# Optimization experiments

Hardware: AMD Instinct MI355X
Metric: run time of the kernel (lower is better)

Reference implementation:

```python
import jax, jax.numpy as jnp
import numpy as np

E = 16          # number of experts
K = 2           # top-k routing
D = 1024        # model dim
F = 512         # expert ffn dim
T = 4096        # tokens
C = 2048


def setup_inputs() -> dict:
    key = jax.random.key(0)
    k1, k2, k3, k4, k5, k6 = jax.random.split(key, 6)
    return {
        "hidden_states": jax.random.normal(k1, (T, D), jnp.float32),
        "topk_indices": jax.random.randint(k2, (T, K), 0, E, jnp.int64),
        "topk_weights": jax.random.uniform(k3, (T, K), jnp.float32),
        "w_gate": jax.random.normal(k4, (E, D, F), jnp.float32) * 0.02,
        "w_up": jax.random.normal(k5, (E, D, F), jnp.float32) * 0.02,
        "w_down": jax.random.normal(k6, (E, F, D), jnp.float32) * 0.02,
    }


def reference(hidden_states, topk_indices, topk_weights, w_gate, w_up, w_down):
    Tn, d = hidden_states.shape
    k = topk_indices.shape[1]
    TK = Tn * k

    # ---- dispatch_tokens: group (token, expert) pairs by expert id ----
    flat_e = topk_indices.reshape(-1)                 # [TK] expert id per slot
    flat_w = topk_weights.reshape(-1)                 # [TK]
    flat_t = jnp.arange(TK) // k                      # [TK] source token id
    order = jnp.argsort(flat_e)                       # sort slots by expert
    se, st, sw = flat_e[order], flat_t[order], flat_w[order]
    counts = jnp.bincount(flat_e, length=E)           # tokens per expert
    starts = jnp.cumsum(counts) - counts              # exclusive prefix sum
    pos = jnp.arange(TK) - starts[se]                 # position within expert bucket
    valid = pos < C
    slot = jnp.where(valid, se * C + pos, E * C)      # overflow -> scratch row

    # gather tokens into padded per-expert buffers [E, C, D]
    buf = jnp.zeros((E * C + 1, d), hidden_states.dtype).at[slot].set(hidden_states[st])
    xe = buf[: E * C].reshape(E, C, d)

    # ---- per-expert gated-SiLU MLP via grouped GEMMs ----
    h = jax.nn.silu(jnp.einsum('ecd,edf->ecf', xe, w_gate)) * jnp.einsum('ecd,edf->ecf', xe, w_up)
    ye = jnp.einsum('ecf,efd->ecd', h, w_down).reshape(E * C, d)

    # ---- weighted scatter-add combine (index_add_) ----
    contrib = ye[jnp.minimum(slot, E * C - 1)] * (sw * valid.astype(sw.dtype))[:, None]
    out = jnp.zeros((Tn, d), topk_weights.dtype).at[st].add(contrib)
    return out.astype(hidden_states.dtype)
```

## Files before the change

### kernel.cpp

```cpp
#include <hip/hip_runtime.h>
#include <hip/hip_bf16.h>

constexpr int E_ = 16, K_ = 2, D_ = 1024, F_ = 512, T_ = 4096;
constexpr int TK_ = T_ * K_;
constexpr int CAP_ = 2048;
constexpr int BM_ = 128;
constexpr int ROWS_MAX = 10240;

constexpr size_t SZ_W   = (size_t)E_ * F_ * D_ * 2;
constexpr size_t OFF_WDT  = 0;
constexpr size_t OFF_WGT  = OFF_WDT + SZ_W;
constexpr size_t OFF_WUT  = OFF_WGT + SZ_W;
constexpr size_t OFF_XG   = OFF_WUT + SZ_W;
constexpr size_t SZ_XG  = (size_t)ROWS_MAX * D_ * 2;
constexpr size_t OFF_H    = OFF_XG + SZ_XG;
constexpr size_t SZ_H   = (size_t)ROWS_MAX * F_ * 2;
constexpr size_t OFF_META = OFF_H + SZ_H;
constexpr size_t OFF_YE   = OFF_WGT;
static_assert(OFF_YE + (size_t)ROWS_MAX * D_ * 4 <= OFF_H, "Ye overlaps live buffers");

typedef __attribute__((ext_vector_type(8))) short short8;
typedef __attribute__((ext_vector_type(4))) float float4v;

__device__ __forceinline__ unsigned short f2bf(float f) {
  union { float f; unsigned int u; } v; v.f = f;
  unsigned int r = (v.u + 0x7fffu + ((v.u >> 16) & 1u)) >> 16;
  return (unsigned short)r;
}

__device__ __forceinline__ void load_lds16(const unsigned short* g, unsigned short* l) {
  __builtin_amdgcn_global_load_lds(
      (const __attribute__((address_space(1))) unsigned int*)g,
      (__attribute__((address_space(3))) unsigned int*)l,
      16, 0, 0);
}

__launch_bounds__(1024)
__global__ void dispatch_k(const int* __restrict__ idx, const float* __restrict__ tw,
                           int* __restrict__ cnt_c, int* __restrict__ off_al,
                           int* __restrict__ row_token, float* __restrict__ row_weight,
                           int* __restrict__ slot_row) {
  __shared__ int hist[E_], offs[E_], ctr[E_];
  int tid = threadIdx.x;
  if (tid < E_) hist[tid] = 0;
  __syncthreads();
  for (int i = tid; i < TK_; i += 1024) atomicAdd(&hist[idx[i]], 1);
  __syncthreads();
  if (tid == 0) {
    int run = 0;
    for (int e = 0; e < E_; ++e) {
      int c = hist[e] > CAP_ ? CAP_ : hist[e];
      cnt_c[e] = c; off_al[e] = run; offs[e] = run; ctr[e] = 0;
      run += (c + BM_ - 1) & ~(BM_ - 1);
    }
  }
  __syncthreads();
  for (int r = tid; r < ROWS_MAX; r += 1024) row_token[r] = -1;
  __syncthreads();
  for (int i = tid; i < TK_; i += 1024) {
    int e = idx[i];
    int r = atomicAdd(&ctr[e], 1);
    int row = -1;
    if (r < CAP_) {
      row = offs[e] + r;
      row_token[row] = i >> 1;
      row_weight[row] = tw[i];
    }
    slot_row[i] = row;
  }
}

__global__ void gather_k(const float* __restrict__ hidden, const int* __restrict__ row_token,
                         unsigned short* __restrict__ Xg) {
  int r = blockIdx.x;
  int tok = row_token[r];
  int c = threadIdx.x * 4;
  ushort4 o;
  if (tok >= 0) {
    float4 v = *(const float4*)(hidden + (size_t)tok * D_ + c);
    o.x = f2bf(v.x); o.y = f2bf(v.y); o.z = f2bf(v.z); o.w = f2bf(v.w);
  } else {
    o.x = 0; o.y = 0; o.z = 0; o.w = 0;
  }
  *(ushort4*)(Xg + (size_t)r * D_ + c) = o;
}

__launch_bounds__(256)
__global__ void transpose_all_k(const float* __restrict__ wg, const float* __restrict__ wu,
                                const float* __restrict__ wd,
                                unsigned short* __restrict__ WgT, unsigned short* __restrict__ WuT,
                                unsigned short* __restrict__ WdT) {
  __shared__ float tile[64][65];
  int z = blockIdx.y;
  int kind = z >> 4, e = z & 15;
  int R = (kind == 2) ? F_ : D_;
  int C = (kind == 2) ? D_ : F_;
  const float* s = ((kind == 0) ? wg : (kind == 1) ? wu : wd) + (size_t)e * R * C;
  unsigned short* d = ((kind == 0) ? WgT : (kind == 1) ? WuT : WdT) + (size_t)e * R * C;
  int tilesX = C >> 6;
  int t = blockIdx.x;
  int r0 = (t / tilesX) * 64, c0 = (t % tilesX) * 64;

  int lr = threadIdx.x >> 4;
  int lc = (threadIdx.x & 15) * 4;
#pragma unroll
  for (int it = 0; it < 4; ++it) {
    int row = lr + it * 16;
    float4 v = *(const float4*)(s + (size_t)(r0 + row) * C + (c0 + lc));
    tile[row][lc + 0] = v.x; tile[row][lc + 1] = v.y;
    tile[row][lc + 2] = v.z; tile[row][lc + 3] = v.w;
  }
  __syncthreads();

  int w = threadIdx.x >> 6, l = threadIdx.x & 63;
#pragma unroll
  for (int it = 0; it < 2; ++it) {
    int c = (it * 4 + w) * 8 + (l >> 3);
    int r8 = (l & 7) * 8;
    short8 o;
#pragma unroll
    for (int j = 0; j < 8; ++j) o[j] = (short)f2bf(tile[r8 + j][c]);
    *(short8*)(d + (size_t)(c0 + c) * R + (r0 + r8)) = o;
  }
}


__launch_bounds__(256)
__global__ void gemm1_k(const unsigned short* __restrict__ Xg,
                        const unsigned short* __restrict__ WgT,
                        const unsigned short* __restrict__ WuT,
                        unsigned short* __restrict__ Hbuf,
                        const int* __restrict__ cnt_c, const int* __restrict__ off_al) {
  int bid = blockIdx.x;
  int swz = (bid & 7) * 512 + (bid >> 3);
  int e = swz >> 8, mt = (swz >> 3) & 31, nt = swz & 7;
  int cnt = cnt_c[e];
  if (mt * 64 >= cnt) return;
  int rbase = off_al[e] + mt * 64;

  __shared__ unsigned short lA[2][64 * 64];
  __shared__ unsigned short lBg[2][64 * 64];
  __shared__ unsigned short lBu[2][64 * 64];

  int tid = threadIdx.x, wid = tid >> 6, lane = tid & 63;
  int wm = wid >> 1, wn = wid & 1;
  int quad = lane >> 4, l15 = lane & 15;
  int sw = l15 & 7;

  const unsigned short* gA = Xg + (size_t)rbase * D_;
  const unsigned short* gB0 = WgT + ((size_t)e * F_ + nt * 64) * D_;
  const unsigned short* gB1 = WuT + ((size_t)e * F_ + nt * 64) * D_;

  float4v accg[2][2], accu[2][2];
#pragma unroll
  for (int i = 0; i < 2; ++i)
#pragma unroll
    for (int j = 0; j < 2; ++j) {
      accg[i][j] = (float4v){0.f, 0.f, 0.f, 0.f};
      accu[i][j] = (float4v){0.f, 0.f, 0.f, 0.f};
    }

  auto stage = [&](int buf, int k0) {
#pragma unroll
    for (int it = 0; it < 2; ++it) {
      int fw = it * 256 + wid * 64;
      int f = fw + lane;
      int row = f >> 3, c8 = (f & 7) ^ (row & 7);
      size_t go = (size_t)row * D_ + k0 + c8 * 8;
      load_lds16(gA + go, &lA[buf][fw * 8]);
      load_lds16(gB0 + go, &lBg[buf][fw * 8]);
      load_lds16(gB1 + go, &lBu[buf][fw * 8]);
    }
  };

  stage(0, 0);
  __syncthreads();

  for (int kt = 0; kt < 16; ++kt) {
    int cur = kt & 1;
    if (kt + 1 < 16) stage(cur ^ 1, (kt + 1) * 64);
#pragma unroll
    for (int kc = 0; kc < 2; ++kc) {
      short8 af[2], bg[2], bu[2];
#pragma unroll
      for (int i = 0; i < 2; ++i) {
        int r = wm * 32 + i * 16 + l15;
        af[i] = *(const short8*)&lA[cur][r * 64 + ((kc * 4 + quad) ^ sw) * 8];
      }
#pragma unroll
      for (int j = 0; j < 2; ++j) {
        int n = wn * 32 + j * 16 + l15;
        bg[j] = *(const short8*)&lBg[cur][n * 64 + ((kc * 4 + quad) ^ sw) * 8];
        bu[j] = *(const short8*)&lBu[cur][n * 64 + ((kc * 4 + quad) ^ sw) * 8];
      }
#pragma unroll
      for (int i = 0; i < 2; ++i)
#pragma unroll
        for (int j = 0; j < 2; ++j) {
          accg[i][j] = __builtin_amdgcn_mfma_f32_16x16x32_bf16(af[i], bg[j], accg[i][j], 0, 0, 0);
          accu[i][j] = __builtin_amdgcn_mfma_f32_16x16x32_bf16(af[i], bu[j], accu[i][j], 0, 0, 0);
        }
    }
    __syncthreads();
  }

  int rem = cnt - mt * 64;
#pragma unroll
  for (int i = 0; i < 2; ++i)
#pragma unroll
    for (int j = 0; j < 2; ++j)
#pragma unroll
      for (int r = 0; r < 4; ++r) {
        int row = wm * 32 + i * 16 + quad * 4 + r;
        if (row < rem) {
          float g = accg[i][j][r], u = accu[i][j][r];
          float h = (g / (1.f + __expf(-g))) * u;
          int n = nt * 64 + wn * 32 + j * 16 + l15;
          Hbuf[(size_t)(rbase + row) * F_ + n] = f2bf(h);
        }
      }
}

__launch_bounds__(256)
__global__ void gemm2_k(const unsigned short* __restrict__ Hbuf,
                        const unsigned short* __restrict__ WdT,
                        float* __restrict__ Ye,
                        const int* __restrict__ cnt_c, const int* __restrict__ off_al) {
  int bid = blockIdx.x;
  int swz = (bid & 7) * 512 + (bid >> 3);
  int e = swz >> 8, mt = (swz >> 3) & 31, nt = swz & 7;
  int cnt = cnt_c[e];
  if (mt * 64 >= cnt) return;
  int rbase = off_al[e] + mt * 64;

  __shared__ unsigned short lA[2][64 * 64];
  __shared__ unsigned short lB[2][128 * 64];

  int tid = threadIdx.x, wid = tid >> 6, lane = tid & 63;
  int wm = wid >> 1, wn = wid & 1;
  int quad = lane >> 4, l15 = lane & 15;
  int sw = l15 & 7;

  const unsigned short* gA = Hbuf + (size_t)rbase * F_;
  const unsigned short* gB = WdT + ((size_t)e * D_ + nt * 128) * F_;

  float4v acc[2][4];
#pragma unroll
  for (int i = 0; i < 2; ++i)
#pragma unroll
    for (int j = 0; j < 4; ++j) acc[i][j] = (float4v){0.f, 0.f, 0.f, 0.f};

  auto stage = [&](int buf, int k0) {
#pragma unroll
    for (int it = 0; it < 2; ++it) {
      int fw = it * 256 + wid * 64;
      int f = fw + lane;
      int row = f >> 3, c8 = (f & 7) ^ (row & 7);
      load_lds16(gA + (size_t)row * F_ + k0 + c8 * 8, &lA[buf][fw * 8]);
    }
#pragma unroll
    for (int it = 0; it < 4; ++it) {
      int fw = it * 256 + wid * 64;
      int f = fw + lane;
      int row = f >> 3, c8 = (f & 7) ^ (row & 7);
      load_lds16(gB + (size_t)row * F_ + k0 + c8 * 8, &lB[buf][fw * 8]);
    }
  };

  stage(0, 0);
  __syncthreads();

  for (int kt = 0; kt < 8; ++kt) {
    int cur = kt & 1;
    if (kt + 1 < 8) stage(cur ^ 1, (kt + 1) * 64);
#pragma unroll
    for (int kc = 0; kc < 2; ++kc) {
      short8 af[2], bf[4];
#pragma unroll
      for (int i = 0; i < 2; ++i) {
        int r = wm * 32 + i * 16 + l15;
        af[i] = *(const short8*)&lA[cur][r * 64 + ((kc * 4 + quad) ^ sw) * 8];
      }
#pragma unroll
      for (int j = 0; j < 4; ++j) {
        int n = wn * 64 + j * 16 + l15;
        bf[j] = *(const short8*)&lB[cur][n * 64 + ((kc * 4 + quad) ^ sw) * 8];
      }
#pragma unroll
      for (int i = 0; i < 2; ++i)
#pragma unroll
        for (int j = 0; j < 4; ++j)
          acc[i][j] = __builtin_amdgcn_mfma_f32_16x16x32_bf16(af[i], bf[j], acc[i][j], 0, 0, 0);
    }
    __syncthreads();
  }

  int rem = cnt - mt * 64;
#pragma unroll
  for (int i = 0; i < 2; ++i)
#pragma unroll
    for (int r = 0; r < 4; ++r) {
      int row = wm * 32 + i * 16 + quad * 4 + r;
      if (row < rem) {
        float* yp = Ye + (size_t)(rbase + row) * D_ + nt * 128 + wn * 64 + l15;
#pragma unroll
        for (int j = 0; j < 4; ++j) yp[j * 16] = acc[i][j][r];
      }
    }
}

__global__ void combine_k(const float* __restrict__ Ye, const int* __restrict__ slot_row,
                          const float* __restrict__ row_weight, float* __restrict__ out) {
  int t = blockIdx.x;
  int c = threadIdx.x * 4;
  int r0 = slot_row[2 * t], r1 = slot_row[2 * t + 1];
  float4 acc = {0.f, 0.f, 0.f, 0.f};
  if (r0 >= 0) {
    float w = row_weight[r0];
    float4 y = *(const float4*)(Ye + (size_t)r0 * D_ + c);
    acc.x = w * y.x; acc.y = w * y.y; acc.z = w * y.z; acc.w = w * y.w;
  }
  if (r1 >= 0) {
    float w = row_weight[r1];
    float4 y = *(const float4*)(Ye + (size_t)r1 * D_ + c);
    acc.x += w * y.x; acc.y += w * y.y; acc.z += w * y.z; acc.w += w * y.w;
  }
  *(float4*)(out + (size_t)t * D_ + c) = acc;
}

extern "C" void kernel_launch(void* const* d_in, const int* in_sizes, int n_in,
                              void* d_out, int out_size, void* d_ws, size_t ws_size,
                              hipStream_t stream) {
  const float* hidden  = (const float*)d_in[0];
  const int*   topkidx = (const int*)d_in[1];
  const float* topkw   = (const float*)d_in[2];
  const float* w_gate  = (const float*)d_in[3];
  const float* w_up    = (const float*)d_in[4];
  const float* w_down  = (const float*)d_in[5];
  float* out = (float*)d_out;

  char* ws = (char*)d_ws;
  unsigned short* WdT = (unsigned short*)(ws + OFF_WDT);
  unsigned short* WgT = (unsigned short*)(ws + OFF_WGT);
  unsigned short* WuT = (unsigned short*)(ws + OFF_WUT);
  unsigned short* Xg  = (unsigned short*)(ws + OFF_XG);
  unsigned short* Hb  = (unsigned short*)(ws + OFF_H);
  float* Ye           = (float*)(ws + OFF_YE);
  int* meta           = (int*)(ws + OFF_META);
  int* cnt_c     = meta;
  int* off_al    = meta + 16;
  int* row_token = meta + 32;
  float* row_weight = (float*)(meta + 32 + ROWS_MAX);
  int* slot_row  = meta + 32 + 2 * ROWS_MAX;

  dispatch_k<<<1, 1024, 0, stream>>>(topkidx, topkw, cnt_c, off_al, row_token, row_weight,
                                     slot_row);
  transpose_all_k<<<dim3(128, 48), 256, 0, stream>>>(w_gate, w_up, w_down, WgT, WuT, WdT);
  gather_k<<<ROWS_MAX, 256, 0, stream>>>(hidden, row_token, Xg);

  gemm1_k<<<4096, 256, 0, stream>>>(Xg, WgT, WuT, Hb, cnt_c, off_al);
  gemm2_k<<<4096, 256, 0, stream>>>(Hb, WdT, Ye, cnt_c, off_al);
  combine_k<<<T_, 256, 0, stream>>>(Ye, slot_row, row_weight, out);
}
```

Measured before the change: 237.5 us.

## Parallelize dispatch across experts and software-pipeline weight transpose tiles

Dispatch now runs one block per expert: each block rebuilds the histogram, computes its own offset, and scans all slots for its expert, so the single-block serial scan is split across 16 blocks. The weight transpose kernel uses 2048 blocks, each handling three tiles, and prefetches the next tile's global loads into registers while the current tile is written out. Rows beyond the padded buffers no longer get -1 written to row_token, so gather now bounds-checks the token index. The per-block ordering within an expert still depends on atomics, and each dispatch block redundantly reads all indices.

```diff
diff --git a/kernel.cpp b/kernel.cpp
--- a/kernel.cpp
+++ b/kernel.cpp
@@ -35,38 +35,44 @@
       16, 0, 0);
 }
 
-__launch_bounds__(1024)
+__launch_bounds__(256)
 __global__ void dispatch_k(const int* __restrict__ idx, const float* __restrict__ tw,
                            int* __restrict__ cnt_c, int* __restrict__ off_al,
                            int* __restrict__ row_token, float* __restrict__ row_weight,
                            int* __restrict__ slot_row) {
-  __shared__ int hist[E_], offs[E_], ctr[E_];
-  int tid = threadIdx.x;
+  __shared__ int hist[E_];
+  __shared__ int off_s, pad_s, cnt_s;
+  int e = blockIdx.x, tid = threadIdx.x;
   if (tid < E_) hist[tid] = 0;
-  __syncthreads();
-  for (int i = tid; i < TK_; i += 1024) atomicAdd(&hist[idx[i]], 1);
+  if (tid == 0) cnt_s = 0;
+  __syncthreads();
+  for (int i = tid; i < TK_; i += 256) atomicAdd(&hist[idx[i]], 1);
   __syncthreads();
   if (tid == 0) {
-    int run = 0;
-    for (int e = 0; e < E_; ++e) {
-      int c = hist[e] > CAP_ ? CAP_ : hist[e];
-      cnt_c[e] = c; off_al[e] = run; offs[e] = run; ctr[e] = 0;
+    int run = 0, off = 0, myc = 0;
+    for (int ee = 0; ee < E_; ++ee) {
+      int c = hist[ee] > CAP_ ? CAP_ : hist[ee];
+      if (ee == e) { off = run; myc = c; }
       run += (c + BM_ - 1) & ~(BM_ - 1);
     }
-  }
-  __syncthreads();
-  for (int r = tid; r < ROWS_MAX; r += 1024) row_token[r] = -1;
-  __syncthreads();
-  for (int i = tid; i < TK_; i += 1024) {
-    int e = idx[i];
-    int r = atomicAdd(&ctr[e], 1);
-    int row = -1;
-    if (r < CAP_) {
-      row = offs[e] + r;
-      row_token[row] = i >> 1;
-      row_weight[row] = tw[i];
-    }
-    slot_row[i] = row;
+    off_s = off; pad_s = (myc + BM_ - 1) & ~(BM_ - 1);
+    cnt_c[e] = myc; off_al[e] = off;
+  }
+  __syncthreads();
+  int off = off_s, pad = pad_s;
+  for (int r = tid; r < pad; r += 256) row_token[off + r] = -1;
+  __syncthreads();
+  for (int i = tid; i < TK_; i += 256) {
+    if (idx[i] == e) {
+      int r = atomicAdd(&cnt_s, 1);
+      int row = -1;
+      if (r < CAP_) {
+        row = off + r;
+        row_token[row] = i >> 1;
+        row_weight[row] = tw[i];
+      }
+      slot_row[i] = row;
+    }
   }
 }
 
@@ -76,7 +82,7 @@
   int tok = row_token[r];
   int c = threadIdx.x * 4;
   ushort4 o;
-  if (tok >= 0) {
+  if ((unsigned)tok < (unsigned)T_) {
     float4 v = *(const float4*)(hidden + (size_t)tok * D_ + c);
     o.x = f2bf(v.x); o.y = f2bf(v.y); o.z = f2bf(v.z); o.w = f2bf(v.w);
   } else {
@@ -91,36 +97,67 @@
                                 unsigned short* __restrict__ WgT, unsigned short* __restrict__ WuT,
                                 unsigned short* __restrict__ WdT) {
   __shared__ float tile[64][65];
-  int z = blockIdx.y;
-  int kind = z >> 4, e = z & 15;
-  int R = (kind == 2) ? F_ : D_;
-  int C = (kind == 2) ? D_ : F_;
-  const float* s = ((kind == 0) ? wg : (kind == 1) ? wu : wd) + (size_t)e * R * C;
-  unsigned short* d = ((kind == 0) ? WgT : (kind == 1) ? WuT : WdT) + (size_t)e * R * C;
-  int tilesX = C >> 6;
-  int t = blockIdx.x;
-  int r0 = (t / tilesX) * 64, c0 = (t % tilesX) * 64;
-
+  int bid = blockIdx.x;
   int lr = threadIdx.x >> 4;
   int lc = (threadIdx.x & 15) * 4;
-#pragma unroll
-  for (int it = 0; it < 4; ++it) {
-    int row = lr + it * 16;
-    float4 v = *(const float4*)(s + (size_t)(r0 + row) * C + (c0 + lc));
-    tile[row][lc + 0] = v.x; tile[row][lc + 1] = v.y;
-    tile[row][lc + 2] = v.z; tile[row][lc + 3] = v.w;
-  }
-  __syncthreads();
-
   int w = threadIdx.x >> 6, l = threadIdx.x & 63;
-#pragma unroll
-  for (int it = 0; it < 2; ++it) {
-    int c = (it * 4 + w) * 8 + (l >> 3);
-    int r8 = (l & 7) * 8;
-    short8 o;
-#pragma unroll
-    for (int j = 0; j < 8; ++j) o[j] = (short)f2bf(tile[r8 + j][c]);
-    *(short8*)(d + (size_t)(c0 + c) * R + (r0 + r8)) = o;
+
+  auto src_of = [&](int g, int& r0, int& c0, int& R_) -> const float* {
+    int z = g >> 7, t = g & 127;
+    int kind = z >> 4, e = z & 15;
+    int R = (kind == 2) ? F_ : D_;
+    int C = (kind == 2) ? D_ : F_;
+    int tilesX = C >> 6;
+    r0 = (t / tilesX) * 64; c0 = (t % tilesX) * 64; R_ = R;
+    return ((kind == 0) ? wg : (kind == 1) ? wu : wd) + (size_t)e * R * C;
+  };
+  auto dst_of = [&](int g) -> unsigned short* {
+    int z = g >> 7;
+    int kind = z >> 4, e = z & 15;
+    size_t n = (size_t)((kind == 2) ? F_ : D_) * ((kind == 2) ? D_ : F_);
+    return ((kind == 0) ? WgT : (kind == 1) ? WuT : WdT) + (size_t)e * n;
+  };
+
+  float4 v[4], v2[4];
+  int r0, c0, R;
+  const float* s = src_of(bid, r0, c0, R);
+  int C = (R == F_) ? D_ : F_;
+#pragma unroll
+  for (int it = 0; it < 4; ++it)
+    v[it] = *(const float4*)(s + (size_t)(r0 + lr + it * 16) * C + (c0 + lc));
+
+#pragma unroll
+  for (int gi = 0; gi < 3; ++gi) {
+    int g = gi * 2048 + bid;
+#pragma unroll
+    for (int it = 0; it < 4; ++it) {
+      int row = lr + it * 16;
+      tile[row][lc + 0] = v[it].x; tile[row][lc + 1] = v[it].y;
+      tile[row][lc + 2] = v[it].z; tile[row][lc + 3] = v[it].w;
+    }
+    int nr0 = 0, nc0 = 0, nR = 0;
+    if (gi < 2) {
+      const float* ns = src_of(g + 2048, nr0, nc0, nR);
+      int nC = (nR == F_) ? D_ : F_;
+#pragma unroll
+      for (int it = 0; it < 4; ++it)
+        v2[it] = *(const float4*)(ns + (size_t)(nr0 + lr + it * 16) * nC + (nc0 + lc));
+    }
+    __syncthreads();
+    unsigned short* d = dst_of(g);
+#pragma unroll
+    for (int it = 0; it < 2; ++it) {
+      int c = (it * 4 + w) * 8 + (l >> 3);
+      int r8 = (l & 7) * 8;
+      short8 o;
+#pragma unroll
+      for (int j = 0; j < 8; ++j) o[j] = (short)f2bf(tile[r8 + j][c]);
+      *(short8*)(d + (size_t)(c0 + c) * R + (r0 + r8)) = o;
+    }
+    __syncthreads();
+    r0 = nr0; c0 = nc0; R = nR;
+#pragma unroll
+    for (int it = 0; it < 4; ++it) v[it] = v2[it];
   }
 }
 
@@ -353,9 +390,9 @@
   float* row_weight = (float*)(meta + 32 + ROWS_MAX);
   int* slot_row  = meta + 32 + 2 * ROWS_MAX;
 
-  dispatch_k<<<1, 1024, 0, stream>>>(topkidx, topkw, cnt_c, off_al, row_token, row_weight,
+  dispatch_k<<<E_, 256, 0, stream>>>(topkidx, topkw, cnt_c, off_al, row_token, row_weight,
                                      slot_row);
-  transpose_all_k<<<dim3(128, 48), 256, 0, stream>>>(w_gate, w_up, w_down, WgT, WuT, WdT);
+  transpose_all_k<<<2048, 256, 0, stream>>>(w_gate, w_up, w_down, WgT, WuT, WdT);
   gather_k<<<ROWS_MAX, 256, 0, stream>>>(hidden, row_token, Xg);
 
   gemm1_k<<<4096, 256, 0, stream>>>(Xg, WgT, WuT, Hb, cnt_c, off_al);
```

Measured after the change: 254.0 us. +6.9%, slower.
